# Kernel tuning notes

Measured on AMD Instinct MI355X. Metric: run time of the kernel, lower is better.

The kernel has to match this reference:

```python
import jax, jax.numpy as jnp
import numpy as np

N, L, C_IN, NOISE_C, COMP, NC = 64, 1024, 514, 64, 16, 3
MAIN_C = COMP + NOISE_C  # 80

def _conv1d(x, w, b):
    # x: [N, Cin, L], w: [Cout, Cin, K] -> 'same' padding conv, stride 1
    k = w.shape[-1]
    y = jax.lax.conv_general_dilated(x, w, (1,), [(k // 2, k // 2)],
                                     dimension_numbers=('NCH', 'OIH', 'NCH'))
    return y + b[None, :, None]

def _bn(x, gamma, beta, eps=1e-5):
    # training-mode BatchNorm1d: biased batch stats over (N, L)
    mu = jnp.mean(x, axis=(0, 2), keepdims=True)
    var = jnp.var(x, axis=(0, 2), keepdims=True)
    return (x - mu) * jax.lax.rsqrt(var + eps) * gamma[None, :, None] + beta[None, :, None]

def _lrelu(x):
    return jax.nn.leaky_relu(x, 0.2)

def _pos_encode(length, dim, dtype):
    d = jnp.arange(dim)
    div = 1.0 / jnp.power(10000.0, (2.0 * (d // 2).astype(dtype)) / dim)  # [dim]
    ang = div[:, None] * jnp.arange(length, dtype=dtype)[None, :]          # [dim, L]
    pe = jnp.where((d % 2 == 0)[:, None], jnp.sin(ang), jnp.cos(ang))
    return pe[None].astype(dtype)  # [1, dim, L]

def _label_revise(probs):
    # Vectorized equivalent of the per-sample Python revision loop
    # (circle_itv=2, slider_itv=4, stride=2). Output length == input length.
    # Row j semantics (m = 4*(j//4), chain(m) = pred[m]==2 and pred[m+4]==2 and m+4<L):
    #   j%4==0: always probs[j]
    #   chain(m) and j%4!=0: pad [0,0,1]
    #   j%4==1 (not chain): pred[m] in {1,2} -> [1,0,0] else probs[j]
    #   j%4==2 (not chain): probs[j]
    #   j%4==3 (not chain): pred[j-1]==1 -> [1,0,0] else probs[j]
    n, l, c = probs.shape
    pred = jnp.argmax(probs, axis=-1)                 # [N, L]
    pred_b = pred[:, ::4]                              # pred at multiples of 4
    nxt = jnp.concatenate([pred_b[:, 1:], jnp.full((n, 1), -1, pred_b.dtype)], axis=1)
    chain = jnp.repeat((pred_b == 2) & (nxt == 2), 4, axis=1)   # [N, L]
    predm = jnp.repeat(pred_b, 4, axis=1)                        # [N, L]
    phase = jnp.arange(l) % 4
    prev = jnp.concatenate([jnp.zeros((n, 1), pred.dtype), pred[:, :-1]], axis=1)
    pad100 = jnp.array([1.0, 0.0, 0.0], probs.dtype)
    pad001 = jnp.array([0.0, 0.0, 1.0], probs.dtype)
    c100 = (((phase == 1)[None] & ((predm == 1) | (predm == 2)))
            | ((phase == 3)[None] & (prev == 1))) & ~chain
    out = jnp.where(c100[..., None], pad100, probs)
    out = jnp.where((chain & (phase != 0)[None])[..., None], pad001, out)
    return out

def _forward(noise, cond_data, gumbel, ew1, eb1, ew2, eb2, eg, ebt,
             w3, b3, w4, b4, g4, bt4, lw1, lb1, lw2, lb2, lw3, lb3):
    # FeatureExtractor
    x = jnp.swapaxes(cond_data, 1, 2)                       # [N, 514, L]
    x = _lrelu(_conv1d(x, ew1, eb1))                        # [N, 32, L]
    cond = _bn(_conv1d(x, ew2, eb2), eg, ebt)               # [N, 16, L] (no act)
    # main generator
    gi = jnp.concatenate([cond, jnp.swapaxes(noise, 1, 2)], axis=1)  # [N, 80, L]
    gi = gi + _pos_encode(L, MAIN_C, gi.dtype)
    h = _lrelu(_conv1d(gi, w3, b3))                         # [N, 48, L]
    h = _lrelu(_bn(_conv1d(h, w4, b4), g4, bt4))            # [N, 12, L]
    h = h.reshape(h.shape[0], -1)                           # [N, 12*L]
    h = _lrelu(h @ lw1 + lb1)
    h = _lrelu(h @ lw2 + lb2)
    logits = (h @ lw3 + lb3).reshape(-1, L, NC)             # [N, L, 3]
    rev = _label_revise(logits)
    # hard gumbel-softmax (tau=1) with straight-through estimator
    y_soft = jax.nn.softmax(rev + gumbel, axis=-1)
    y_hard = jax.nn.one_hot(jnp.argmax(y_soft, axis=-1), NC, dtype=y_soft.dtype)
    gen = y_hard + y_soft - jax.lax.stop_gradient(y_soft)
    return gen, cond

def setup_inputs() -> dict:
    key = jax.random.key(0)
    ks = jax.random.split(key, 12)
    s = jnp.float32(0.02)
    return {
        'noise': jax.random.normal(ks[0], (N, L, NOISE_C), jnp.float32),
        'cond_data': jax.random.normal(ks[1], (N, L, C_IN), jnp.float32),
        'gumbel': jax.random.gumbel(ks[2], (N, L, NC), jnp.float32),
        'ew1': jax.random.normal(ks[3], (C_IN // 16, C_IN, 1), jnp.float32) * s,
        'eb1': jnp.zeros((C_IN // 16,), jnp.float32),
        'ew2': jax.random.normal(ks[4], (COMP, C_IN // 16, 3), jnp.float32) * s,
        'eb2': jnp.zeros((COMP,), jnp.float32),
        'eg': jnp.ones((COMP,), jnp.float32),
        'ebt': jnp.zeros((COMP,), jnp.float32),
        'w3': jax.random.normal(ks[5], (NC * 16, MAIN_C, 7), jnp.float32) * s,
        'b3': jnp.zeros((NC * 16,), jnp.float32),
        'w4': jax.random.normal(ks[6], (NC * 4, NC * 16, 3), jnp.float32) * s,
        'b4': jnp.zeros((NC * 4,), jnp.float32),
        'g4': jnp.ones((NC * 4,), jnp.float32),
        'bt4': jnp.zeros((NC * 4,), jnp.float32),
        'lw1': jax.random.normal(ks[7], (NC * 4 * L, NC * L), jnp.float32) * s,
        'lb1': jnp.zeros((NC * L,), jnp.float32),
        'lw2': jax.random.normal(ks[8], (NC * L, NC * L), jnp.float32) * s,
        'lb2': jnp.zeros((NC * L,), jnp.float32),
        'lw3': jax.random.normal(ks[9], (NC * L, NC * L), jnp.float32) * s,
        'lb3': jnp.zeros((NC * L,), jnp.float32),
    }

def reference(noise, cond_data, gumbel, ew1, eb1, ew2, eb2, eg, ebt,
              w3, b3, w4, b4, g4, bt4, lw1, lb1, lw2, lb2, lw3, lb3):
    return _forward(noise, cond_data, gumbel, ew1, eb1, ew2, eb2, eg, ebt,
                    w3, b3, w4, b4, g4, bt4, lw1, lb1, lw2, lb2, lw3, lb3)
```

## Files before the change

### kernel.cpp

```cpp
#include <hip/hip_runtime.h>
#include <hip/hip_bf16.h>
#include <math.h>


__device__ __forceinline__ float lrelu(float x){ return fmaxf(x, 0.2f*x); }

__global__ void k_init(const float* __restrict__ ew1, const float* __restrict__ ew2,
                       const float* __restrict__ w3,  const float* __restrict__ w4,
                       float* __restrict__ wT1, float* __restrict__ wT2,
                       float* __restrict__ wT3, float* __restrict__ wT4,
                       float* __restrict__ pe){
  int i = blockIdx.x*256 + threadIdx.x;
  if (i < 16448){
    int c = i>>5, oc = i&31;
    wT1[i] = ew1[oc*514 + c];
  } else if (i < 16448+1536){
    int j = i - 16448; int oc = j%16; int t = j/16; int dl = t%3; int ic = t/3;
    wT2[j] = ew2[(oc*32+ic)*3 + dl];
  } else if (i < 16448+1536+26880){
    int j = i - 17984; int oc = j%48; int t = j/48; int dl = t%7; int ic = t/7;
    wT3[j] = w3[(oc*80+ic)*7 + dl];
  } else if (i < 46592){
    int j = i - 44864; int oc = j%12; int t = j/12; int dl = t%3; int ic = t/3;
    wT4[j] = w4[(oc*48+ic)*3 + dl];
  } else if (i < 46592 + 80*1024){
    int j = i - 46592;
    int ch = j >> 10, l = j & 1023;
    double dv = 1.0 / pow(10000.0, (2.0*(double)(ch>>1)) / 80.0);
    double ang = dv * (double)l;
    pe[j] = (float)((ch & 1) ? cos(ang) : sin(ang));
  }
}

__global__ __launch_bounds__(256) void k_conv1(const float* __restrict__ A,
    const float* __restrict__ wT1, const float* __restrict__ eb1,
    float* __restrict__ x1){
  __shared__ float red[32][256];
  const int tid = threadIdx.x;
  const int pl  = tid & 63;
  const int s   = __builtin_amdgcn_readfirstlane(tid >> 6);
  const int p   = blockIdx.x*64 + pl;

  const int c0 = (s == 0) ? 0 : 130 + (s-1)*128;
  const int c1 = (s == 0) ? 130 : 130 + s*128;

  const float* row = A + (size_t)p*514;
  float acc[32];
  #pragma unroll
  for (int j=0;j<32;j++) acc[j]=0.f;

  #pragma unroll 8
  for (int c=c0;c<c1;c+=2){
    float2 v = *reinterpret_cast<const float2*>(row + c);
    const float* w = wT1 + (size_t)c*32;
    #pragma unroll
    for (int j=0;j<32;j++) acc[j] = fmaf(v.x, w[j],    acc[j]);
    #pragma unroll
    for (int j=0;j<32;j++) acc[j] = fmaf(v.y, w[32+j], acc[j]);
  }

  #pragma unroll
  for (int j=0;j<32;j++) red[j][s*64 + pl] = acc[j];
  __syncthreads();

  float out[8];
  #pragma unroll
  for (int j=0;j<8;j++){
    const int c = s*8 + j;
    float v = (red[c][pl] + red[c][64+pl]) + (red[c][128+pl] + red[c][192+pl]);
    out[j] = lrelu(v + eb1[c]);
  }
  float* dst = x1 + ((size_t)(blockIdx.x*64 + pl))*32 + s*8;
  *(float4*)(dst  ) = make_float4(out[0],out[1],out[2],out[3]);
  *(float4*)(dst+4) = make_float4(out[4],out[5],out[6],out[7]);
}

__global__ __launch_bounds__(256) void k_conv2(const float* __restrict__ x1,
    const float* __restrict__ wT2, const float* __restrict__ eb2,
    float* __restrict__ y2, float* __restrict__ part){
  __shared__ float xt[32][264];
  const int tid = threadIdx.x, lane = tid & 63;
  const int wv = __builtin_amdgcn_readfirstlane(tid >> 6);
  const int n = blockIdx.x >> 2, base = (blockIdx.x & 3)*256;

  for (int r = tid; r < 264; r += 256){
    int l = base - 4 + r;
    if (l >= 0 && l < 1024){
      const float* src = x1 + ((size_t)n*1024 + l)*32;
      #pragma unroll
      for (int c=0;c<32;c+=4){
        float4 v = *(const float4*)(src + c);
        xt[c][r]=v.x; xt[c+1][r]=v.y; xt[c+2][r]=v.z; xt[c+3][r]=v.w;
      }
    } else {
      #pragma unroll
      for (int c=0;c<32;c++) xt[c][r] = 0.f;
    }
  }
  __syncthreads();

  const int og = wv*4;
  const int j0 = 4*lane;
  float acc[4][4];
  #pragma unroll
  for (int j=0;j<4;j++){
    #pragma unroll
    for (int p=0;p<4;p++) acc[j][p]=0.f;
  }
  for (int ic=0; ic<32; ic++){
    float xr[12];
    #pragma unroll
    for (int u=0;u<12;u+=4){
      float4 v = *(const float4*)&xt[ic][j0+u];
      xr[u]=v.x; xr[u+1]=v.y; xr[u+2]=v.z; xr[u+3]=v.w;
    }
    const float* wrow = wT2 + ic*48 + og;
    #pragma unroll
    for (int dl=0;dl<3;dl++){
      #pragma unroll
      for (int j=0;j<4;j++){
        float w = wrow[dl*16 + j];
        #pragma unroll
        for (int p=0;p<4;p++)
          acc[j][p] = fmaf(xr[p+dl+3], w, acc[j][p]);
      }
    }
  }
  float s[4], q[4];
  #pragma unroll
  for (int j=0;j<4;j++){ s[j]=0.f; q[j]=0.f; }
  const int l0 = base + 4*lane;
  #pragma unroll
  for (int p=0;p<4;p++){
    float vv[4];
    #pragma unroll
    for (int j=0;j<4;j++){
      float val = acc[j][p] + eb2[og+j];
      vv[j]=val; s[j]+=val; q[j]+=val*val;
    }
    *(float4*)(y2 + ((size_t)n*1024 + l0 + p)*16 + og) = make_float4(vv[0],vv[1],vv[2],vv[3]);
  }
  #pragma unroll
  for (int off=32; off; off>>=1){
    #pragma unroll
    for (int j=0;j<4;j++){ s[j] += __shfl_xor(s[j], off); q[j] += __shfl_xor(q[j], off); }
  }
  if (lane == 0){
    #pragma unroll
    for (int j=0;j<4;j++){
      part[((size_t)blockIdx.x*16 + og + j)*2    ] = s[j];
      part[((size_t)blockIdx.x*16 + og + j)*2 + 1] = q[j];
    }
  }
}

__global__ __launch_bounds__(256) void k_conv3(const float* __restrict__ y2,
    const float* __restrict__ noise, const float* __restrict__ pe,
    const float* __restrict__ bn2p, const float* __restrict__ eg,
    const float* __restrict__ ebt,
    const float* __restrict__ wT3, const float* __restrict__ b3,
    float* __restrict__ h3, float* __restrict__ cond_out){
  __shared__ float xt[80][72];
  __shared__ double pS[16][16], pQ[16][16];
  __shared__ float ssh[32];
  const int tid = threadIdx.x, lane = tid & 63;
  const int og = __builtin_amdgcn_readfirstlane(tid >> 6) * 12;
  const int n = blockIdx.x >> 4, base = (blockIdx.x & 15)*64;

  {
    int c = tid & 15, chunk = tid >> 4;
    double S=0.0, Q=0.0;
    #pragma unroll 4
    for (int i=chunk*16; i<chunk*16+16; i++){
      S += (double)bn2p[((size_t)i*16 + c)*2];
      Q += (double)bn2p[((size_t)i*16 + c)*2 + 1];
    }
    pS[chunk][c] = S; pQ[chunk][c] = Q;
  }
  __syncthreads();
  if (tid < 16){
    double S=0.0, Q=0.0;
    #pragma unroll
    for (int k=0;k<16;k++){ S += pS[k][tid]; Q += pQ[k][tid]; }
    double mean = S / 65536.0;
    double var  = Q / 65536.0 - mean*mean;
    double sc   = (double)eg[tid] / sqrt(var + 1e-5);
    ssh[tid*2]   = (float)sc;
    ssh[tid*2+1] = (float)((double)ebt[tid] - mean*sc);
  }
  __syncthreads();

  {
    const int q = tid & 3;
    for (int r = tid >> 2; r < 72; r += 64){
      int l = base - 4 + r;
      bool valid = (l >= 0 && l < 1024);
      if (q == 0){
        if (valid){
          size_t p = (size_t)n*1024 + l;
          const float* ys = y2 + p*16;
          bool interior = (r >= 4 && r < 68);
          #pragma unroll
          for (int c=0;c<16;c++){
            float cv = fmaf(ys[c], ssh[2*c], ssh[2*c+1]);
            if (interior) cond_out[((size_t)n*16 + c)*1024 + l] = cv;
            xt[c][r] = cv + pe[c*1024 + l];
          }
          const float* ns = noise + p*64;
          #pragma unroll
          for (int c=0;c<4;c++)
            xt[16+c][r] = ns[c] + pe[(16+c)*1024 + l];
        } else {
          #pragma unroll
          for (int c=0;c<20;c++) xt[c][r] = 0.f;
        }
      } else {
        if (valid){
          size_t p = (size_t)n*1024 + l;
          const float* ns = noise + p*64 + (q*20 - 16);
          #pragma unroll
          for (int c=0;c<20;c++)
            xt[q*20 + c][r] = ns[c] + pe[(q*20 + c)*1024 + l];
        } else {
          #pragma unroll
          for (int c=0;c<20;c++) xt[q*20 + c][r] = 0.f;
        }
      }
    }
  }
  __syncthreads();

  float acc[12];
  #pragma unroll
  for (int j=0;j<12;j++) acc[j]=0.f;
  for (int ic=0; ic<80; ic++){
    float xr[7];
    #pragma unroll
    for (int u=0;u<7;u++) xr[u] = xt[ic][lane+1+u];
    const float* wrow = wT3 + ic*336 + og;
    #pragma unroll
    for (int dl=0;dl<7;dl++){
      #pragma unroll
      for (int j=0;j<12;j++)
        acc[j] = fmaf(xr[dl], wrow[dl*48 + j], acc[j]);
    }
  }
  {
    float v[12];
    #pragma unroll
    for (int j=0;j<12;j++) v[j] = lrelu(acc[j] + b3[og+j]);
    float* dst = h3 + ((size_t)n*1024 + base + lane)*48 + og;
    *(float4*)(dst  ) = make_float4(v[0],v[1],v[2],v[3]);
    *(float4*)(dst+4) = make_float4(v[4],v[5],v[6],v[7]);
    *(float4*)(dst+8) = make_float4(v[8],v[9],v[10],v[11]);
  }
}

__global__ __launch_bounds__(256) void k_conv4(const float* __restrict__ h3,
    const float* __restrict__ wT4, const float* __restrict__ b4,
    float* __restrict__ y4, float* __restrict__ part){
  __shared__ float xt[48][258];
  __shared__ float red[4][24];
  const int tid = threadIdx.x, lane = tid & 63, wv = tid >> 6;
  const int n = blockIdx.x >> 2, base = (blockIdx.x & 3)*256;

  for (int r = tid; r < 258; r += 256){
    int l = base - 1 + r;
    if (l >= 0 && l < 1024){
      const float* src = h3 + ((size_t)n*1024 + l)*48;
      #pragma unroll
      for (int c=0;c<48;c+=4){
        float4 v = *(const float4*)(src + c);
        xt[c][r]=v.x; xt[c+1][r]=v.y; xt[c+2][r]=v.z; xt[c+3][r]=v.w;
      }
    } else {
      #pragma unroll
      for (int c=0;c<48;c++) xt[c][r]=0.f;
    }
  }
  __syncthreads();

  float acc[12];
  #pragma unroll
  for (int j=0;j<12;j++) acc[j]=0.f;
  for (int ic=0; ic<48; ic++){
    float x0 = xt[ic][tid], x1v = xt[ic][tid+1], x2 = xt[ic][tid+2];
    const float* wrow = wT4 + ic*36;
    #pragma unroll
    for (int j=0;j<12;j++){
      acc[j] = fmaf(x0,  wrow[j],      acc[j]);
      acc[j] = fmaf(x1v, wrow[12 + j], acc[j]);
      acc[j] = fmaf(x2,  wrow[24 + j], acc[j]);
    }
  }
  float s[12], q[12];
  #pragma unroll
  for (int j=0;j<12;j++){
    float v = acc[j] + b4[j];
    acc[j] = v; s[j] = v; q[j] = v*v;
  }
  {
    float* dst = y4 + ((size_t)n*1024 + base + tid)*12;
    *(float4*)(dst  ) = make_float4(acc[0],acc[1],acc[2],acc[3]);
    *(float4*)(dst+4) = make_float4(acc[4],acc[5],acc[6],acc[7]);
    *(float4*)(dst+8) = make_float4(acc[8],acc[9],acc[10],acc[11]);
  }
  #pragma unroll
  for (int off=32; off; off>>=1){
    #pragma unroll
    for (int j=0;j<12;j++){ s[j] += __shfl_xor(s[j], off); q[j] += __shfl_xor(q[j], off); }
  }
  if (lane == 0){
    #pragma unroll
    for (int j=0;j<12;j++){ red[wv][j] = s[j]; red[wv][12+j] = q[j]; }
  }
  __syncthreads();
  if (tid < 24){
    float v = red[0][tid] + red[1][tid] + red[2][tid] + red[3][tid];
    if (tid < 12) part[((size_t)blockIdx.x*12 + tid)*2] = v;
    else          part[((size_t)blockIdx.x*12 + (tid-12))*2 + 1] = v;
  }
}

__global__ __launch_bounds__(256) void k_hflat(const float* __restrict__ y4,
    const float* __restrict__ bn4p, const float* __restrict__ g4,
    const float* __restrict__ bt4, float* __restrict__ hT){
  __shared__ double pS[16][12], pQ[16][12];
  __shared__ float ssh[24];
  const int tid = threadIdx.x;
  if (tid < 192){
    int c = tid % 12, chunk = tid / 12;
    double S=0.0, Q=0.0;
    #pragma unroll 4
    for (int i=chunk*16; i<chunk*16+16; i++){
      S += (double)bn4p[((size_t)i*12 + c)*2];
      Q += (double)bn4p[((size_t)i*12 + c)*2 + 1];
    }
    pS[chunk][c] = S; pQ[chunk][c] = Q;
  }
  __syncthreads();
  if (tid < 12){
    double S=0.0, Q=0.0;
    #pragma unroll
    for (int k=0;k<16;k++){ S += pS[k][tid]; Q += pQ[k][tid]; }
    double mean = S / 65536.0;
    double var  = Q / 65536.0 - mean*mean;
    double sc   = (double)g4[tid] / sqrt(var + 1e-5);
    ssh[tid*2]   = (float)sc;
    ssh[tid*2+1] = (float)((double)bt4[tid] - mean*sc);
  }
  __syncthreads();

  int nn = tid & 63;
  int l  = blockIdx.x*4 + (tid >> 6);
  const float* src = y4 + ((size_t)nn*1024 + l)*12;
  #pragma unroll
  for (int c=0;c<12;c++){
    float v = lrelu(fmaf(src[c], ssh[2*c], ssh[2*c+1]));
    hT[((size_t)(c*1024 + l))*64 + nn] = v;
  }
}

__global__ __launch_bounds__(256) void k_fc2(const float* __restrict__ AT,
    const float* __restrict__ W, float* __restrict__ part,
    int nsplit, int kwave){
  __shared__ float red[64][64];
  const int lane = threadIdx.x & 63;
  const int w  = __builtin_amdgcn_readfirstlane(threadIdx.x >> 6);
  const int sk = w >> 1;
  const int mh = (w & 1) * 32;
  const int s  = blockIdx.x % nsplit;
  const int ot = blockIdx.x / nsplit;
  const int o  = ot*64 + lane;
  const int k0 = (s*2 + sk) * kwave;

  float acc[32];
  #pragma unroll
  for (int m=0;m<32;m++) acc[m]=0.f;

  const float* ap = AT + (size_t)k0*64 + mh;
  const float* wp = W  + (size_t)k0*3072 + o;

  float wb[16];
  #pragma unroll
  for (int u=0;u<16;u++) wb[u] = wp[(size_t)u*3072];

  for (int k=0; k<kwave-16; k+=16){
    float wn[16];
    const float* wpn = wp + (size_t)(k+16)*3072;
    #pragma unroll
    for (int u=0;u<16;u++) wn[u] = wpn[(size_t)u*3072];
    #pragma unroll
    for (int u=0;u<16;u++){
      const float* a = ap + (size_t)(k+u)*64;
      #pragma unroll
      for (int m=0;m<32;m++) acc[m] = fmaf(a[m], wb[u], acc[m]);
    }
    #pragma unroll
    for (int u=0;u<16;u++) wb[u] = wn[u];
  }
  #pragma unroll
  for (int u=0;u<16;u++){
    const float* a = ap + (size_t)(kwave-16+u)*64;
    #pragma unroll
    for (int m=0;m<32;m++) acc[m] = fmaf(a[m], wb[u], acc[m]);
  }

  if (sk == 1){
    #pragma unroll
    for (int m=0;m<32;m++) red[mh + m][lane] = acc[m];
  }
  __syncthreads();
  if (sk == 0){
    float* dst = part + (size_t)s*64*3072 + o;
    #pragma unroll
    for (int m=0;m<32;m++){
      acc[m] += red[mh + m][lane];
      dst[(size_t)(mh + m)*3072] = acc[m];
    }
  }
}

__global__ __launch_bounds__(256) void k_fcreduce(const float* __restrict__ part,
    const float* __restrict__ bias, float* __restrict__ out,
    int S, int act, int transposed){
  const int ot = blockIdx.x >> 4;
  const int mg = blockIdx.x & 15;
  const int lane = threadIdx.x & 63;
  const int o = ot*64 + lane;
  const int m = mg*4 + (threadIdx.x >> 6);
  float v = 0.f;
  for (int s=0;s<S;s++) v += part[((size_t)s*64 + m)*3072 + o];
  v += bias[o];
  if (act) v = fmaxf(v, 0.2f*v);
  if (transposed) out[(size_t)o*64 + m] = v;
  else            out[(size_t)m*3072 + o] = v;
}

__global__ __launch_bounds__(256) void k_label(const float* __restrict__ logits,
    const float* __restrict__ gumbel, float* __restrict__ out){
  __shared__ int pred[1024];
  const int n = blockIdx.x;
  const float* lg = logits + (size_t)n*3072;
  for (int l = threadIdx.x; l < 1024; l += 256){
    float a = lg[l*3], b = lg[l*3+1], c = lg[l*3+2];
    int pm = 0; float bv = a;
    if (b > bv){ pm = 1; bv = b; }
    if (c > bv){ pm = 2; }
    pred[l] = pm;
  }
  __syncthreads();
  const float* gm = gumbel + (size_t)n*3072;
  float* op = out + (size_t)n*3072;
  for (int l = threadIdx.x; l < 1024; l += 256){
    int phase = l & 3, lb = l >> 2;
    int pb  = pred[lb*4];
    int nxt = (lb < 255) ? pred[(lb+1)*4] : -1;
    bool chain = (pb == 2) && (nxt == 2);
    int prev = (l > 0) ? pred[l-1] : 0;
    bool c100 = (((phase == 1) && (pb == 1 || pb == 2)) ||
                 ((phase == 3) && (prev == 1))) && !chain;
    float r0, r1, r2;
    if (chain && phase != 0){ r0=0.f; r1=0.f; r2=1.f; }
    else if (c100)          { r0=1.f; r1=0.f; r2=0.f; }
    else { r0 = lg[l*3]; r1 = lg[l*3+1]; r2 = lg[l*3+2]; }
    float z0 = r0 + gm[l*3], z1 = r1 + gm[l*3+1], z2 = r2 + gm[l*3+2];
    int am = 0; float bv = z0;
    if (z1 > bv){ am = 1; bv = z1; }
    if (z2 > bv){ am = 2; }
    op[l*3+0] = (am == 0) ? 1.f : 0.f;
    op[l*3+1] = (am == 1) ? 1.f : 0.f;
    op[l*3+2] = (am == 2) ? 1.f : 0.f;
  }
}

extern "C" void kernel_launch(void* const* d_in, const int* in_sizes, int n_in,
                              void* d_out, int out_size, void* d_ws, size_t ws_size,
                              hipStream_t stream){
  (void)in_sizes; (void)n_in; (void)out_size;
  const float* noise     = (const float*)d_in[0];
  const float* cond_data = (const float*)d_in[1];
  const float* gumbel    = (const float*)d_in[2];
  const float* ew1 = (const float*)d_in[3];
  const float* eb1 = (const float*)d_in[4];
  const float* ew2 = (const float*)d_in[5];
  const float* eb2 = (const float*)d_in[6];
  const float* eg  = (const float*)d_in[7];
  const float* ebt = (const float*)d_in[8];
  const float* w3  = (const float*)d_in[9];
  const float* b3  = (const float*)d_in[10];
  const float* w4  = (const float*)d_in[11];
  const float* b4  = (const float*)d_in[12];
  const float* g4  = (const float*)d_in[13];
  const float* bt4 = (const float*)d_in[14];
  const float* lw1 = (const float*)d_in[15];
  const float* lb1 = (const float*)d_in[16];
  const float* lw2 = (const float*)d_in[17];
  const float* lb2 = (const float*)d_in[18];
  const float* lw3 = (const float*)d_in[19];
  const float* lb3 = (const float*)d_in[20];

  float* ws = (float*)d_ws;
  float* wT1   = ws + 0;
  float* wT2   = ws + 16448;
  float* wT3   = ws + 17984;
  float* wT4   = ws + 44864;
  float* pe    = ws + 46592;
  float* bn2p  = ws + 128512;
  float* bn4p  = ws + 136736;
  float* x1    = ws + 143360;
  float* y2    = ws + 2240512;
  float* h3    = ws + 3289088;
  float* y4    = ws + 6434816;
  float* hT    = ws + 7221248;
  float* fcp   = ws + 8007680;

  int S1 = 32;
  if (ws_size < (size_t)(8007680 + 32*196608 + 3*196608) * 4) S1 = 16;
  const int S23 = 16;
  float* fc1T  = fcp + (size_t)S1*196608;
  float* fc2T  = fc1T + 196608;
  float* logi  = fc2T + 196608;
  const int kw1  = 12288 / (S1*2);
  const int kw23 = 3072 / (S23*2);

  float* out_gen  = (float*)d_out;
  float* out_cond = (float*)d_out + 196608;

  k_init <<<502, 256, 0, stream>>>(ew1, ew2, w3, w4, wT1, wT2, wT3, wT4, pe);
  k_conv1<<<1024, 256, 0, stream>>>(cond_data, wT1, eb1, x1);
  k_conv2<<<256, 256, 0, stream>>>(x1, wT2, eb2, y2, bn2p);
  k_conv3<<<1024, 256, 0, stream>>>(y2, noise, pe, bn2p, eg, ebt, wT3, b3, h3, out_cond);
  k_conv4<<<256, 256, 0, stream>>>(h3, wT4, b4, y4, bn4p);
  k_hflat<<<256, 256, 0, stream>>>(y4, bn4p, g4, bt4, hT);
  k_fc2  <<<48*S1, 256, 0, stream>>>(hT,   lw1, fcp, S1, kw1);
  k_fcreduce<<<768, 256, 0, stream>>>(fcp, lb1, fc1T, S1, 1, 1);
  k_fc2  <<<48*S23, 256, 0, stream>>>(fc1T, lw2, fcp, S23, kw23);
  k_fcreduce<<<768, 256, 0, stream>>>(fcp, lb2, fc2T, S23, 1, 1);
  k_fc2  <<<48*S23, 256, 0, stream>>>(fc2T, lw3, fcp, S23, kw23);
  k_fcreduce<<<768, 256, 0, stream>>>(fcp, lb3, logi, S23, 0, 0);
  k_label<<<64, 256, 0, stream>>>(logi, gumbel, out_gen);
}
```

Measured before the change: 360.1 us.

## Stage FC activation tiles in double-buffered LDS with vectorized loads

The FC GEMV-like kernel now stages 16-row chunks of the transposed activation matrix into a double-buffered shared-memory tile with cooperative float4 loads. The inner product reads activations as float4 from LDS instead of scalar global loads. Weight prefetch depth drops from 16 to 8 rows per group. This targets the per-lane scalar global reads of activations, which every wave re-fetched. The cost is an extra barrier per chunk, and the code assumes kwave is a multiple of 16.

```diff
diff --git a/kernel.cpp b/kernel.cpp
--- a/kernel.cpp
+++ b/kernel.cpp
@@ -364,9 +364,10 @@
 __global__ __launch_bounds__(256) void k_fc2(const float* __restrict__ AT,
     const float* __restrict__ W, float* __restrict__ part,
     int nsplit, int kwave){
-  __shared__ float red[64][64];
-  const int lane = threadIdx.x & 63;
-  const int w  = __builtin_amdgcn_readfirstlane(threadIdx.x >> 6);
+  __shared__ float lds[4096];
+  const int tid  = threadIdx.x;
+  const int lane = tid & 63;
+  const int w  = __builtin_amdgcn_readfirstlane(tid >> 6);
   const int sk = w >> 1;
   const int mh = (w & 1) * 32;
   const int s  = blockIdx.x % nsplit;
@@ -374,49 +375,86 @@
   const int o  = ot*64 + lane;
   const int k0 = (s*2 + sk) * kwave;
 
+  const int st_sk  = tid >> 7;
+  const int st_row = (tid >> 3) & 15;
+  const int st_m   = (tid & 7) * 8;
+  const float* ast = AT + ((size_t)(s*2 + st_sk)*kwave + st_row)*64 + st_m;
+  const int st_off = st_sk*1024 + st_row*64 + st_m;
+
   float acc[32];
   #pragma unroll
   for (int m=0;m<32;m++) acc[m]=0.f;
 
-  const float* ap = AT + (size_t)k0*64 + mh;
-  const float* wp = W  + (size_t)k0*3072 + o;
-
-  float wb[16];
-  #pragma unroll
-  for (int u=0;u<16;u++) wb[u] = wp[(size_t)u*3072];
-
-  for (int k=0; k<kwave-16; k+=16){
-    float wn[16];
-    const float* wpn = wp + (size_t)(k+16)*3072;
-    #pragma unroll
-    for (int u=0;u<16;u++) wn[u] = wpn[(size_t)u*3072];
-    #pragma unroll
-    for (int u=0;u<16;u++){
-      const float* a = ap + (size_t)(k+u)*64;
-      #pragma unroll
-      for (int m=0;m<32;m++) acc[m] = fmaf(a[m], wb[u], acc[m]);
-    }
-    #pragma unroll
-    for (int u=0;u<16;u++) wb[u] = wn[u];
-  }
-  #pragma unroll
-  for (int u=0;u<16;u++){
-    const float* a = ap + (size_t)(kwave-16+u)*64;
-    #pragma unroll
-    for (int m=0;m<32;m++) acc[m] = fmaf(a[m], wb[u], acc[m]);
+  const float* wp = W + (size_t)k0*3072 + o;
+  float wb[8];
+  #pragma unroll
+  for (int u=0;u<8;u++) wb[u] = wp[(size_t)u*3072];
+
+  {
+    float4 v0 = *(const float4*)(ast);
+    float4 v1 = *(const float4*)(ast + 4);
+    *(float4*)(lds + st_off)     = v0;
+    *(float4*)(lds + st_off + 4) = v1;
+  }
+  __syncthreads();
+
+  const int nch = kwave >> 4;
+  const int a_base = sk*1024 + mh;
+
+  for (int c = 0; c < nch; ++c){
+    const int buf = (c & 1) << 11;
+    float4 n0, n1;
+    if (c+1 < nch){
+      const float* asrc = ast + (size_t)(c+1)*1024;
+      n0 = *(const float4*)(asrc);
+      n1 = *(const float4*)(asrc + 4);
+    }
+    #pragma unroll
+    for (int g=0; g<2; ++g){
+      const int kk = c*16 + g*8;
+      float wn[8];
+      const bool pref = (kk + 8 < kwave);
+      if (pref){
+        const float* wpn = wp + (size_t)(kk+8)*3072;
+        #pragma unroll
+        for (int u=0;u<8;u++) wn[u] = wpn[(size_t)u*3072];
+      }
+      #pragma unroll
+      for (int u=0;u<8;u++){
+        const float* arow = lds + buf + a_base + (g*8+u)*64;
+        #pragma unroll
+        for (int i=0;i<8;i++){
+          float4 av = *(const float4*)(arow + i*4);
+          acc[i*4+0] = fmaf(av.x, wb[u], acc[i*4+0]);
+          acc[i*4+1] = fmaf(av.y, wb[u], acc[i*4+1]);
+          acc[i*4+2] = fmaf(av.z, wb[u], acc[i*4+2]);
+          acc[i*4+3] = fmaf(av.w, wb[u], acc[i*4+3]);
+        }
+      }
+      if (pref){
+        #pragma unroll
+        for (int u=0;u<8;u++) wb[u] = wn[u];
+      }
+    }
+    if (c+1 < nch){
+      float* d = lds + (((c+1) & 1) << 11) + st_off;
+      *(float4*)(d)     = n0;
+      *(float4*)(d + 4) = n1;
+    }
+    __syncthreads();
   }
 
   if (sk == 1){
     #pragma unroll
-    for (int m=0;m<32;m++) red[mh + m][lane] = acc[m];
+    for (int m=0;m<32;m++) lds[(mh+m)*64 + lane] = acc[m];
   }
   __syncthreads();
   if (sk == 0){
     float* dst = part + (size_t)s*64*3072 + o;
     #pragma unroll
     for (int m=0;m<32;m++){
-      acc[m] += red[mh + m][lane];
-      dst[(size_t)(mh + m)*3072] = acc[m];
+      acc[m] += lds[(mh+m)*64 + lane];
+      dst[(size_t)(mh+m)*3072] = acc[m];
     }
   }
 }
```

Measured after the change: 944.1 us. 162% more time.

## Remap FC GEMM so lanes own batch rows and weights broadcast per wave

Applied to the files above, without the earlier changes.

Replaces the FC split-K kernel. Each lane used to own one output column and read the activation matrix per row; now each lane owns one batch row and each wave handles 16 output columns, reading uniform weight rows as broadcast loads. The in-block LDS reduction of two K halves is removed, so each block covers one K chunk of doubled length. The partial layout becomes [split][out][batch], so the reduce kernels are rewritten, and the final non-transposed reduce now transposes through shared memory. The change targets the heavy streaming of the large FC weights, but weight loads become 16 scalar-like reads per row, and both occupancy and coalescing change.

```diff
diff --git a/kernel.cpp b/kernel.cpp
--- a/kernel.cpp
+++ b/kernel.cpp
@@ -361,80 +361,69 @@
   }
 }
 
-__global__ __launch_bounds__(256) void k_fc2(const float* __restrict__ AT,
+__global__ __launch_bounds__(256) void k_fc3(const float* __restrict__ AT,
     const float* __restrict__ W, float* __restrict__ part,
     int nsplit, int kwave){
-  __shared__ float red[64][64];
   const int lane = threadIdx.x & 63;
-  const int w  = __builtin_amdgcn_readfirstlane(threadIdx.x >> 6);
-  const int sk = w >> 1;
-  const int mh = (w & 1) * 32;
+  const int wv = __builtin_amdgcn_readfirstlane(threadIdx.x >> 6);
   const int s  = blockIdx.x % nsplit;
   const int ot = blockIdx.x / nsplit;
-  const int o  = ot*64 + lane;
-  const int k0 = (s*2 + sk) * kwave;
-
-  float acc[32];
-  #pragma unroll
-  for (int m=0;m<32;m++) acc[m]=0.f;
-
-  const float* ap = AT + (size_t)k0*64 + mh;
-  const float* wp = W  + (size_t)k0*3072 + o;
-
-  float wb[16];
-  #pragma unroll
-  for (int u=0;u<16;u++) wb[u] = wp[(size_t)u*3072];
-
-  for (int k=0; k<kwave-16; k+=16){
-    float wn[16];
-    const float* wpn = wp + (size_t)(k+16)*3072;
-    #pragma unroll
-    for (int u=0;u<16;u++) wn[u] = wpn[(size_t)u*3072];
-    #pragma unroll
-    for (int u=0;u<16;u++){
-      const float* a = ap + (size_t)(k+u)*64;
-      #pragma unroll
-      for (int m=0;m<32;m++) acc[m] = fmaf(a[m], wb[u], acc[m]);
-    }
-    #pragma unroll
-    for (int u=0;u<16;u++) wb[u] = wn[u];
-  }
-  #pragma unroll
-  for (int u=0;u<16;u++){
-    const float* a = ap + (size_t)(kwave-16+u)*64;
-    #pragma unroll
-    for (int m=0;m<32;m++) acc[m] = fmaf(a[m], wb[u], acc[m]);
-  }
-
-  if (sk == 1){
-    #pragma unroll
-    for (int m=0;m<32;m++) red[mh + m][lane] = acc[m];
-  }
-  __syncthreads();
-  if (sk == 0){
-    float* dst = part + (size_t)s*64*3072 + o;
-    #pragma unroll
-    for (int m=0;m<32;m++){
-      acc[m] += red[mh + m][lane];
-      dst[(size_t)(mh + m)*3072] = acc[m];
-    }
-  }
-}
-
-__global__ __launch_bounds__(256) void k_fcreduce(const float* __restrict__ part,
-    const float* __restrict__ bias, float* __restrict__ out,
-    int S, int act, int transposed){
-  const int ot = blockIdx.x >> 4;
-  const int mg = blockIdx.x & 15;
-  const int lane = threadIdx.x & 63;
-  const int o = ot*64 + lane;
-  const int m = mg*4 + (threadIdx.x >> 6);
+  const int ob = ot*64 + wv*16;
+  const int k0 = s * kwave;
+
+  float acc[16];
+  #pragma unroll
+  for (int j=0;j<16;j++) acc[j]=0.f;
+
+  const float* ap = AT + (size_t)k0*64 + lane;
+  const float* wp = W  + (size_t)k0*3072 + ob;
+
+  #pragma unroll 4
+  for (int k=0;k<kwave;k++){
+    float a = ap[(size_t)k*64];
+    const float* wr = wp + (size_t)k*3072;
+    #pragma unroll
+    for (int j=0;j<16;j++) acc[j] = fmaf(a, wr[j], acc[j]);
+  }
+
+  float* dst = part + ((size_t)s*3072 + ob)*64 + lane;
+  #pragma unroll
+  for (int j=0;j<16;j++) dst[(size_t)j*64] = acc[j];
+}
+
+__global__ __launch_bounds__(256) void k_fcreduce_t1(const float* __restrict__ part,
+    const float* __restrict__ bias, float* __restrict__ out, int S){
+  const int m = threadIdx.x & 63;
+  const int o = blockIdx.x*4 + (threadIdx.x >> 6);
   float v = 0.f;
-  for (int s=0;s<S;s++) v += part[((size_t)s*64 + m)*3072 + o];
+  for (int s=0;s<S;s++) v += part[((size_t)s*3072 + o)*64 + m];
   v += bias[o];
-  if (act) v = fmaxf(v, 0.2f*v);
-  if (transposed) out[(size_t)o*64 + m] = v;
-  else            out[(size_t)m*3072 + o] = v;
+  v = fmaxf(v, 0.2f*v);
+  out[(size_t)o*64 + m] = v;
+}
+
+__global__ __launch_bounds__(256) void k_fcreduce_t0(const float* __restrict__ part,
+    const float* __restrict__ bias, float* __restrict__ out, int S){
+  __shared__ float t[64][65];
+  const int tid = threadIdx.x;
+  const int ob = blockIdx.x*64;
+  {
+    const int m = tid & 63, og = tid >> 6;
+    for (int i=0;i<16;i++){
+      int ol = og*16 + i;
+      float v = 0.f;
+      for (int s=0;s<S;s++) v += part[((size_t)s*3072 + ob + ol)*64 + m];
+      t[ol][m] = v + bias[ob+ol];
+    }
+  }
+  __syncthreads();
+  {
+    const int ol = tid & 63, mg = tid >> 6;
+    for (int i=0;i<16;i++){
+      int m = mg*16 + i;
+      out[(size_t)m*3072 + ob + ol] = t[ol][m];
+    }
+  }
 }
 
 __global__ __launch_bounds__(256) void k_label(const float* __restrict__ logits,
@@ -521,8 +510,8 @@
   float* fc1T  = fcp + (size_t)S1*196608;
   float* fc2T  = fc1T + 196608;
   float* logi  = fc2T + 196608;
-  const int kw1  = 12288 / (S1*2);
-  const int kw23 = 3072 / (S23*2);
+  const int kw1  = 12288 / S1;
+  const int kw23 = 3072 / S23;
 
   float* out_gen  = (float*)d_out;
   float* out_cond = (float*)d_out + 196608;
@@ -533,11 +522,11 @@
   k_conv3<<<1024, 256, 0, stream>>>(y2, noise, pe, bn2p, eg, ebt, wT3, b3, h3, out_cond);
   k_conv4<<<256, 256, 0, stream>>>(h3, wT4, b4, y4, bn4p);
   k_hflat<<<256, 256, 0, stream>>>(y4, bn4p, g4, bt4, hT);
-  k_fc2  <<<48*S1, 256, 0, stream>>>(hT,   lw1, fcp, S1, kw1);
-  k_fcreduce<<<768, 256, 0, stream>>>(fcp, lb1, fc1T, S1, 1, 1);
-  k_fc2  <<<48*S23, 256, 0, stream>>>(fc1T, lw2, fcp, S23, kw23);
-  k_fcreduce<<<768, 256, 0, stream>>>(fcp, lb2, fc2T, S23, 1, 1);
-  k_fc2  <<<48*S23, 256, 0, stream>>>(fc2T, lw3, fcp, S23, kw23);
-  k_fcreduce<<<768, 256, 0, stream>>>(fcp, lb3, logi, S23, 0, 0);
+  k_fc3  <<<48*S1, 256, 0, stream>>>(hT,   lw1, fcp, S1, kw1);
+  k_fcreduce_t1<<<768, 256, 0, stream>>>(fcp, lb1, fc1T, S1);
+  k_fc3  <<<48*S23, 256, 0, stream>>>(fc1T, lw2, fcp, S23, kw23);
+  k_fcreduce_t1<<<768, 256, 0, stream>>>(fcp, lb2, fc2T, S23);
+  k_fc3  <<<48*S23, 256, 0, stream>>>(fc2T, lw3, fcp, S23, kw23);
+  k_fcreduce_t0<<<48, 256, 0, stream>>>(fcp, lb3, logi, S23);
   k_label<<<64, 256, 0, stream>>>(logi, gumbel, out_gen);
 }
```

Result: slower. 449.9 us (+24.9%).
